# Kernel optimization log

Measured on AMD Instinct MI355X. Metric: run time of the kernel, lower is better.

## Reference

```python
import jax, jax.numpy as jnp
import numpy as np
import math

D_MODEL = 768
ED = 768           # d_inner = expand_factor * d_model = 768
N_STATE = 1        # ssm d_state
DT_RANK = math.ceil(D_MODEL / 16)  # 48
EPS = 1e-6


def setup_inputs() -> dict:
    key = jax.random.key(0)
    ks = jax.random.split(key, 12)
    s = lambda k, shape, scale: jax.random.normal(k, shape, dtype=jnp.float32) * scale
    x = jax.random.normal(ks[0], (8, 4096, D_MODEL), dtype=jnp.float32)
    return {
        "x": x,
        "rms_w": jnp.ones((D_MODEL,), jnp.float32),
        "in_proj_w": s(ks[1], (2 * ED, D_MODEL), 0.02),
        "conv_w": s(ks[2], (ED,), 0.5),          # depthwise conv, kernel=1 -> per-channel scale
        "conv_b": s(ks[3], (ED,), 0.02),
        "x_proj_w": s(ks[4], (DT_RANK + 2 * N_STATE, ED), 0.02),
        "dt_proj_w": s(ks[5], (ED, DT_RANK), 0.02),
        "dt_proj_b": s(ks[6], (ED,), 0.02),
        "A_log": jnp.log(jnp.tile(jnp.arange(1, N_STATE + 1, dtype=jnp.float32), (ED, 1))),  # (ED, N)
        "D": jnp.ones((ED,), jnp.float32),
        "out_proj_w": s(ks[7], (D_MODEL, ED), 0.02),
    }


def _selective_scan(xc, delta, A, Bm, C, D):
    # xc: (B,L,ED), delta: (B,L,ED), A: (ED,N), Bm: (B,L,N), C: (B,L,N)
    deltaA = jnp.exp(delta[..., None] * A)                      # (B,L,ED,N)
    deltaBx = delta[..., None] * Bm[:, :, None, :] * xc[..., None]  # (B,L,ED,N)

    def combine(left, right):
        a1, b1 = left
        a2, b2 = right
        return a1 * a2, a2 * b1 + b2

    _, hs = jax.lax.associative_scan(combine, (deltaA, deltaBx), axis=1)  # hs: (B,L,ED,N)
    y = jnp.einsum('blen,bln->ble', hs, C) + D * xc
    return y


def reference(x, rms_w, in_proj_w, conv_w, conv_b, x_proj_w, dt_proj_w,
              dt_proj_b, A_log, D, out_proj_w):
    # RMSNorm
    xn = x * jax.lax.rsqrt(jnp.mean(x * x, axis=-1, keepdims=True) + EPS) * rms_w

    # MambaBlock
    xz = xn @ in_proj_w.T                    # (B,L,2*ED)
    xc, z = jnp.split(xz, 2, axis=-1)
    # depthwise conv1d with kernel_size=1, padding=0 -> per-channel affine
    xc = jax.nn.silu(xc * conv_w + conv_b)

    dbc = xc @ x_proj_w.T                    # (B,L,dt_rank+2N)
    delta = dbc[..., :DT_RANK]
    Bm = dbc[..., DT_RANK:DT_RANK + N_STATE]
    C = dbc[..., DT_RANK + N_STATE:]
    delta = jax.nn.softplus(delta @ dt_proj_w.T + dt_proj_b)  # (B,L,ED)

    A = -jnp.exp(A_log)                      # (ED,N)
    y = _selective_scan(xc, delta, A, Bm, C, D)
    y = y * jax.nn.silu(z)
    return y @ out_proj_w.T                  # (B,L,D_MODEL)
```

## Files before the change

kernel.cpp:

```cpp
#include <hip/hip_runtime.h>

#define TOK   32768
#define DM    768
#define KDIM  768
#define LSEQ  4096
#define NC    64
#define CL    64
#define NCHAIN 6144

typedef __bf16 bf16x8 __attribute__((ext_vector_type(8)));
typedef float  f32x4  __attribute__((ext_vector_type(4)));
typedef unsigned short u16;
typedef unsigned int u32;

__device__ __forceinline__ u16 f2bf(float f) {
  unsigned u = __builtin_bit_cast(unsigned, f);
  u += 0x7fffu + ((u >> 16) & 1u);
  return (u16)(u >> 16);
}
__device__ __forceinline__ float bf2f(u32 h) {
  unsigned u = (h & 0xffffu) << 16;
  return __builtin_bit_cast(float, u);
}

#define GLOAD_LDS16(g, l) __builtin_amdgcn_global_load_lds( \
    (const __attribute__((address_space(1))) void*)(g),     \
    (__attribute__((address_space(3))) void*)(l), 16, 0, 0)

__global__ void cvt_k(const float* __restrict__ src, u16* __restrict__ dst, int n) {
  int i = blockIdx.x * 256 + threadIdx.x;
  if (i < n) dst[i] = f2bf(src[i]);
}

__global__ void cvt_pad_k(const float* __restrict__ src, u16* __restrict__ dst,
                          int rows, int cols, int dcols, int n) {
  int i = blockIdx.x * 256 + threadIdx.x;
  if (i >= n) return;
  int r = i / dcols, c = i % dcols;
  dst[i] = (r < rows && c < cols) ? f2bf(src[r * cols + c]) : (u16)0;
}

__global__ __launch_bounds__(192)
void rmsnorm_k(const float* __restrict__ x, const float* __restrict__ w,
               u16* __restrict__ xnb) {
  long t = blockIdx.x;
  int tid = threadIdx.x;
  float4 v = ((const float4*)x)[t * 192 + tid];
  float s = v.x * v.x + v.y * v.y + v.z * v.z + v.w * v.w;
#pragma unroll
  for (int o = 32; o; o >>= 1) s += __shfl_down(s, o, 64);
  __shared__ float red[3];
  if ((tid & 63) == 0) red[tid >> 6] = s;
  __syncthreads();
  float sc = rsqrtf((red[0] + red[1] + red[2]) * (1.f / 768.f) + 1e-6f);
  float4 ww = ((const float4*)w)[tid];
  ushort4 o;
  o.x = f2bf(v.x * sc * ww.x);
  o.y = f2bf(v.y * sc * ww.y);
  o.z = f2bf(v.z * sc * ww.z);
  o.w = f2bf(v.w * sc * ww.w);
  ((ushort4*)xnb)[t * 192 + tid] = o;
}

template <int EPI>
__global__ __launch_bounds__(256)
void gemm32(const u16* __restrict__ A, int lda,
            const u16* __restrict__ B, int ldb, int K,
            int GX, int RPX,
            float* __restrict__ C,
            const float* __restrict__ w0, const float* __restrict__ w1,
            u16* __restrict__ o0, u16* __restrict__ o1) {
  __shared__ __align__(16) u16 smA[2 * 4096];
  __shared__ __align__(16) u16 smB[2 * 4096];
  const int tid = threadIdx.x;
  const int lane = tid & 63;
  const int wid = tid >> 6;

  const int bid = blockIdx.x;
  const int xcd = bid & 7;
  const int p = bid >> 3;
  const int colp = p % GX;
  const int rowp = xcd * RPX + p / GX;
  const long rowBase = (long)rowp * 128;
  const long colBase = (long)colp * 128;

  const int wr = (wid >> 1) * 64;
  const int wc = (wid & 1) * 64;
  const int lr = lane & 15;
  const int kc = lane >> 4;
  const int kcs = kc ^ ((lr >> 1) & 3);

  const int c1 = tid + 256;
  const u16* gA0 = A + (rowBase + (tid >> 2)) * lda + ((tid & 3) ^ ((tid >> 3) & 3)) * 8;
  const u16* gA1 = A + (rowBase + (c1 >> 2)) * lda + ((c1 & 3) ^ ((c1 >> 3) & 3)) * 8;
  const u16* gB0 = B + (colBase + (tid >> 2)) * ldb + ((tid & 3) ^ ((tid >> 3) & 3)) * 8;
  const u16* gB1 = B + (colBase + (c1 >> 2)) * ldb + ((c1 & 3) ^ ((c1 >> 3) & 3)) * 8;

  f32x4 acc[4][4] = {};
  const int NT = K >> 5;

  auto STAGE = [&](int buf, int kt) {
    u16* bA = smA + buf * 4096;
    u16* bB = smB + buf * 4096;
    GLOAD_LDS16(gA0 + kt, &bA[tid * 8]);
    GLOAD_LDS16(gA1 + kt, &bA[c1 * 8]);
    GLOAD_LDS16(gB0 + kt, &bB[tid * 8]);
    GLOAD_LDS16(gB1 + kt, &bB[c1 * 8]);
  };

  STAGE(0, 0);
  __syncthreads();

  for (int t = 0; t < NT; ++t) {
    if (t + 1 < NT) STAGE((t + 1) & 1, (t + 1) << 5);
    const u16* cA = smA + (t & 1) * 4096;
    const u16* cB = smB + (t & 1) * 4096;
    bf16x8 af[4], bfr[4];
#pragma unroll
    for (int m = 0; m < 4; ++m)
      af[m] = *(const bf16x8*)&cA[(wr + m * 16 + lr) * 32 + kcs * 8];
#pragma unroll
    for (int n = 0; n < 4; ++n)
      bfr[n] = *(const bf16x8*)&cB[(wc + n * 16 + lr) * 32 + kcs * 8];
#pragma unroll
    for (int m = 0; m < 4; ++m)
#pragma unroll
      for (int n = 0; n < 4; ++n)
        acc[m][n] = __builtin_amdgcn_mfma_f32_16x16x32_bf16(af[m], bfr[n], acc[m][n], 0, 0, 0);
    __syncthreads();
  }

#pragma unroll
  for (int m = 0; m < 4; ++m)
#pragma unroll
    for (int n = 0; n < 4; ++n)
#pragma unroll
      for (int j = 0; j < 4; ++j) {
        long grow = rowBase + wr + m * 16 + kc * 4 + j;
        long gcol = colBase + wc + n * 16 + lr;
        float v = acc[m][n][j];
        if (EPI == 0) {
          C[grow * DM + gcol] = v;
        } else if (EPI == 1) {
          if (gcol < DM) {
            float t = v * w0[gcol] + w1[gcol];
            o0[grow * DM + gcol] = f2bf(t / (1.f + __expf(-t)));
          } else {
            o1[grow * DM + (gcol - DM)] = f2bf(v / (1.f + __expf(-v)));
          }
        } else if (EPI == 2) {
          float t = v + w0[gcol];
          float d = (t > 20.f) ? t : __logf(1.f + __expf(t));
          o0[grow * DM + gcol] = f2bf(d);
        } else {
          if (gcol < 64) o0[grow * 64 + gcol] = f2bf(v);
          if (gcol == 48) C[grow * 2 + 0] = v;
          if (gcol == 49) C[grow * 2 + 1] = v;
        }
      }
}

__global__ __launch_bounds__(384)
void scan1_k(const u16* __restrict__ deltab, const u16* __restrict__ xcb,
             const float* __restrict__ bmc, const float* __restrict__ A_log,
             float* __restrict__ aprod, float* __restrict__ hend) {
  int pe = threadIdx.x;
  int b = blockIdx.x, c = blockIdx.y;
  int e0 = pe * 2;
  float Ae0 = -__expf(A_log[e0]), Ae1 = -__expf(A_log[e0 + 1]);
  float ap0 = 1.f, h0 = 0.f, ap1 = 1.f, h1 = 0.f;
  long base = (long)b * LSEQ + (long)c * CL;
  for (int i = 0; i < CL; ++i) {
    long t = base + i;
    u32 dv = *(const u32*)&deltab[t * DM + e0];
    u32 xv = *(const u32*)&xcb[t * DM + e0];
    float Bm = bmc[t * 2];
    float d0 = bf2f(dv), d1 = bf2f(dv >> 16);
    float x0 = bf2f(xv), x1 = bf2f(xv >> 16);
    float a0 = __expf(d0 * Ae0), a1 = __expf(d1 * Ae1);
    ap0 *= a0; h0 = a0 * h0 + d0 * Bm * x0;
    ap1 *= a1; h1 = a1 * h1 + d1 * Bm * x1;
  }
  long chain = (long)c * NCHAIN + b * DM + e0;
  *(float2*)&aprod[chain] = make_float2(ap0, ap1);
  *(float2*)&hend[chain]  = make_float2(h0, h1);
}

__global__ __launch_bounds__(256)
void scan2_k(const float* __restrict__ aprod, const float* __restrict__ hend,
             float* __restrict__ carry) {
  int chain = blockIdx.x * 256 + threadIdx.x;
  float h = 0.f;
  for (int c = 0; c < NC; ++c) {
    carry[c * NCHAIN + chain] = h;
    h = aprod[c * NCHAIN + chain] * h + hend[c * NCHAIN + chain];
  }
}

__global__ __launch_bounds__(384)
void scan3_k(const u16* __restrict__ deltab, const u16* __restrict__ xcb,
             const float* __restrict__ bmc, const float* __restrict__ A_log,
             const float* __restrict__ Dp, const u16* __restrict__ szb,
             const float* __restrict__ carry, u16* __restrict__ ybf) {
  int pe = threadIdx.x;
  int b = blockIdx.x, c = blockIdx.y;
  int e0 = pe * 2;
  float Ae0 = -__expf(A_log[e0]), Ae1 = -__expf(A_log[e0 + 1]);
  float De0 = Dp[e0], De1 = Dp[e0 + 1];
  long chain = (long)c * NCHAIN + b * DM + e0;
  float2 hc = *(const float2*)&carry[chain];
  float h0 = hc.x, h1 = hc.y;
  long base = (long)b * LSEQ + (long)c * CL;
  for (int i = 0; i < CL; ++i) {
    long t = base + i;
    u32 dv = *(const u32*)&deltab[t * DM + e0];
    u32 xv = *(const u32*)&xcb[t * DM + e0];
    u32 sv = *(const u32*)&szb[t * DM + e0];
    float Bm = bmc[t * 2], Cc = bmc[t * 2 + 1];
    float d0 = bf2f(dv), d1 = bf2f(dv >> 16);
    float x0 = bf2f(xv), x1 = bf2f(xv >> 16);
    float a0 = __expf(d0 * Ae0), a1 = __expf(d1 * Ae1);
    h0 = a0 * h0 + d0 * Bm * x0;
    h1 = a1 * h1 + d1 * Bm * x1;
    float y0 = (h0 * Cc + De0 * x0) * bf2f(sv);
    float y1 = (h1 * Cc + De1 * x1) * bf2f(sv >> 16);
    *(u32*)&ybf[t * DM + e0] = (u32)f2bf(y0) | ((u32)f2bf(y1) << 16);
  }
}

extern "C" void kernel_launch(void* const* d_in, const int* in_sizes, int n_in,
                              void* d_out, int out_size, void* d_ws, size_t ws_size,
                              hipStream_t stream) {
  const float* x         = (const float*)d_in[0];
  const float* rms_w     = (const float*)d_in[1];
  const float* in_proj_w = (const float*)d_in[2];
  const float* conv_w    = (const float*)d_in[3];
  const float* conv_b    = (const float*)d_in[4];
  const float* x_proj_w  = (const float*)d_in[5];
  const float* dt_proj_w = (const float*)d_in[6];
  const float* dt_proj_b = (const float*)d_in[7];
  const float* A_log     = (const float*)d_in[8];
  const float* Dp        = (const float*)d_in[9];
  const float* out_proj_w= (const float*)d_in[10];
  float* out = (float*)d_out;

  char* ws = (char*)d_ws;
  size_t off = 0;
  auto alloc = [&](size_t bytes) -> void* {
    void* p = ws + off;
    off += (bytes + 255) & ~(size_t)255;
    return p;
  };
  u16*   xnb    = (u16*)alloc((size_t)TOK * DM * 2);
  u16*   xcb    = (u16*)alloc((size_t)TOK * DM * 2);
  u16*   szb    = (u16*)alloc((size_t)TOK * DM * 2);
  u16*   ybf    = (u16*)alloc((size_t)TOK * DM * 2);
  u16*   deltab = (u16*)alloc((size_t)TOK * DM * 2);
  u16*   dbcb   = (u16*)alloc((size_t)TOK * 64 * 2);
  float* bmc    = (float*)alloc((size_t)TOK * 2 * 4);
  u16*   wInB   = (u16*)alloc((size_t)1536 * 768 * 2);
  u16*   wXpB   = (u16*)alloc((size_t)128 * 768 * 2);
  u16*   wDtB   = (u16*)alloc((size_t)768 * 64 * 2);
  u16*   wOutB  = (u16*)alloc((size_t)768 * 768 * 2);
  float* aprod  = (float*)alloc((size_t)NC * NCHAIN * 4);
  float* hend   = (float*)alloc((size_t)NC * NCHAIN * 4);
  float* carry  = (float*)alloc((size_t)NC * NCHAIN * 4);

  cvt_k<<<(1536 * 768 + 255) / 256, 256, 0, stream>>>(in_proj_w, wInB, 1536 * 768);
  cvt_k<<<(768 * 768 + 255) / 256, 256, 0, stream>>>(out_proj_w, wOutB, 768 * 768);
  cvt_pad_k<<<(128 * 768 + 255) / 256, 256, 0, stream>>>(x_proj_w, wXpB, 50, 768, 768, 128 * 768);
  cvt_pad_k<<<(768 * 64 + 255) / 256, 256, 0, stream>>>(dt_proj_w, wDtB, 768, 48, 64, 768 * 64);

  rmsnorm_k<<<TOK, 192, 0, stream>>>(x, rms_w, xnb);

  gemm32<1><<<3072, 256, 0, stream>>>(
      xnb, DM, wInB, DM, KDIM, 12, 32, nullptr, conv_w, conv_b, xcb, szb);

  gemm32<3><<<256, 256, 0, stream>>>(
      xcb, DM, wXpB, DM, KDIM, 1, 32, bmc, nullptr, nullptr, dbcb, nullptr);

  gemm32<2><<<1536, 256, 0, stream>>>(
      dbcb, 64, wDtB, 64, 64, 6, 32, nullptr, dt_proj_b, nullptr, deltab, nullptr);

  scan1_k<<<dim3(8, NC), 384, 0, stream>>>(deltab, xcb, bmc, A_log, aprod, hend);
  scan2_k<<<NCHAIN / 256, 256, 0, stream>>>(aprod, hend, carry);
  scan3_k<<<dim3(8, NC), 384, 0, stream>>>(deltab, xcb, bmc, A_log, Dp, szb, carry, ybf);

  gemm32<0><<<1536, 256, 0, stream>>>(
      ybf, DM, wOutB, DM, KDIM, 6, 32, out, nullptr, nullptr, nullptr, nullptr);
}
```

Measured before the change: 343.9 us.

## Replace 4-wave GEMM with single-wave 64x64 tiles and barrier-free pipelining

Rewrites the shared GEMM kernel so each block is one 64-thread wavefront computing a 64x64 tile, not four waves on a 128x128 tile. Because a single wave owns its LDS tiles, __syncthreads is dropped and replaced with explicit vmcnt/lgkmcnt waits. Loads are issued two k-steps ahead, with the next stage overwriting the buffer just read. This removes block-level barrier stalls and adds parallelism, at the cost of less data reuse per tile (more global/L2 traffic) and many more small blocks. The grid sizes for all four GEMM launches are rescaled to match.

```diff
diff --git a/kernel.cpp b/kernel.cpp
--- a/kernel.cpp
+++ b/kernel.cpp
@@ -63,71 +63,66 @@
 }
 
 template <int EPI>
-__global__ __launch_bounds__(256)
-void gemm32(const u16* __restrict__ A, int lda,
-            const u16* __restrict__ B, int ldb, int K,
-            int GX, int RPX,
-            float* __restrict__ C,
-            const float* __restrict__ w0, const float* __restrict__ w1,
-            u16* __restrict__ o0, u16* __restrict__ o1) {
-  __shared__ __align__(16) u16 smA[2 * 4096];
-  __shared__ __align__(16) u16 smB[2 * 4096];
-  const int tid = threadIdx.x;
-  const int lane = tid & 63;
-  const int wid = tid >> 6;
-
+__global__ __launch_bounds__(64)
+void gemmw(const u16* __restrict__ A, int lda,
+           const u16* __restrict__ B, int ldb, int K,
+           int GX, int RPX,
+           float* __restrict__ C,
+           const float* __restrict__ w0, const float* __restrict__ w1,
+           u16* __restrict__ o0, u16* __restrict__ o1) {
+  __shared__ __align__(16) u16 smA[2 * 2048];
+  __shared__ __align__(16) u16 smB[2 * 2048];
+  const int l = threadIdx.x;
   const int bid = blockIdx.x;
   const int xcd = bid & 7;
   const int p = bid >> 3;
-  const int colp = p % GX;
-  const int rowp = xcd * RPX + p / GX;
-  const long rowBase = (long)rowp * 128;
-  const long colBase = (long)colp * 128;
-
-  const int wr = (wid >> 1) * 64;
-  const int wc = (wid & 1) * 64;
-  const int lr = lane & 15;
-  const int kc = lane >> 4;
+  const long rowBase = (long)(xcd * RPX + p / GX) * 64;
+  const long colBase = (long)(p % GX) * 64;
+
+  const int lr = l & 15;
+  const int kc = l >> 4;
   const int kcs = kc ^ ((lr >> 1) & 3);
 
-  const int c1 = tid + 256;
-  const u16* gA0 = A + (rowBase + (tid >> 2)) * lda + ((tid & 3) ^ ((tid >> 3) & 3)) * 8;
-  const u16* gA1 = A + (rowBase + (c1 >> 2)) * lda + ((c1 & 3) ^ ((c1 >> 3) & 3)) * 8;
-  const u16* gB0 = B + (colBase + (tid >> 2)) * ldb + ((tid & 3) ^ ((tid >> 3) & 3)) * 8;
-  const u16* gB1 = B + (colBase + (c1 >> 2)) * ldb + ((c1 & 3) ^ ((c1 >> 3) & 3)) * 8;
+  const int srow = l >> 2;
+  const int sslot = (l & 3) ^ ((l >> 3) & 3);
+  const u16* gA = A + (rowBase + srow) * lda + sslot * 8;
+  const u16* gB = B + (colBase + srow) * ldb + sslot * 8;
 
   f32x4 acc[4][4] = {};
   const int NT = K >> 5;
 
   auto STAGE = [&](int buf, int kt) {
-    u16* bA = smA + buf * 4096;
-    u16* bB = smB + buf * 4096;
-    GLOAD_LDS16(gA0 + kt, &bA[tid * 8]);
-    GLOAD_LDS16(gA1 + kt, &bA[c1 * 8]);
-    GLOAD_LDS16(gB0 + kt, &bB[tid * 8]);
-    GLOAD_LDS16(gB1 + kt, &bB[c1 * 8]);
+    u16* bA = smA + buf * 2048;
+    u16* bB = smB + buf * 2048;
+#pragma unroll
+    for (int i = 0; i < 4; ++i) {
+      GLOAD_LDS16(gA + (long)(16 * i) * lda + kt, &bA[(l + 64 * i) * 8]);
+      GLOAD_LDS16(gB + (long)(16 * i) * ldb + kt, &bB[(l + 64 * i) * 8]);
+    }
   };
 
   STAGE(0, 0);
-  __syncthreads();
+  if (NT > 1) STAGE(1, 32);
 
   for (int t = 0; t < NT; ++t) {
-    if (t + 1 < NT) STAGE((t + 1) & 1, (t + 1) << 5);
-    const u16* cA = smA + (t & 1) * 4096;
-    const u16* cB = smB + (t & 1) * 4096;
+    if (t + 1 < NT) asm volatile("s_waitcnt vmcnt(8)" ::: "memory");
+    else            asm volatile("s_waitcnt vmcnt(0)" ::: "memory");
+    const u16* cA = smA + (t & 1) * 2048;
+    const u16* cB = smB + (t & 1) * 2048;
     bf16x8 af[4], bfr[4];
 #pragma unroll
     for (int m = 0; m < 4; ++m)
-      af[m] = *(const bf16x8*)&cA[(wr + m * 16 + lr) * 32 + kcs * 8];
+      af[m] = *(const bf16x8*)&cA[(m * 16 + lr) * 32 + kcs * 8];
 #pragma unroll
     for (int n = 0; n < 4; ++n)
-      bfr[n] = *(const bf16x8*)&cB[(wc + n * 16 + lr) * 32 + kcs * 8];
+      bfr[n] = *(const bf16x8*)&cB[(n * 16 + lr) * 32 + kcs * 8];
+    asm volatile("s_waitcnt lgkmcnt(0)" ::: "memory");
+    if (t + 2 < NT) STAGE(t & 1, (t + 2) << 5);
 #pragma unroll
     for (int m = 0; m < 4; ++m)
 #pragma unroll
       for (int n = 0; n < 4; ++n)
         acc[m][n] = __builtin_amdgcn_mfma_f32_16x16x32_bf16(af[m], bfr[n], acc[m][n], 0, 0, 0);
-    __syncthreads();
   }
 
 #pragma unroll
@@ -136,24 +131,24 @@
     for (int n = 0; n < 4; ++n)
 #pragma unroll
       for (int j = 0; j < 4; ++j) {
-        long grow = rowBase + wr + m * 16 + kc * 4 + j;
-        long gcol = colBase + wc + n * 16 + lr;
+        long grow = rowBase + m * 16 + kc * 4 + j;
+        long gcol = colBase + n * 16 + lr;
         float v = acc[m][n][j];
         if (EPI == 0) {
           C[grow * DM + gcol] = v;
         } else if (EPI == 1) {
           if (gcol < DM) {
-            float t = v * w0[gcol] + w1[gcol];
-            o0[grow * DM + gcol] = f2bf(t / (1.f + __expf(-t)));
+            float t2 = v * w0[gcol] + w1[gcol];
+            o0[grow * DM + gcol] = f2bf(t2 / (1.f + __expf(-t2)));
           } else {
             o1[grow * DM + (gcol - DM)] = f2bf(v / (1.f + __expf(-v)));
           }
         } else if (EPI == 2) {
-          float t = v + w0[gcol];
-          float d = (t > 20.f) ? t : __logf(1.f + __expf(t));
+          float t2 = v + w0[gcol];
+          float d = (t2 > 20.f) ? t2 : __logf(1.f + __expf(t2));
           o0[grow * DM + gcol] = f2bf(d);
         } else {
-          if (gcol < 64) o0[grow * 64 + gcol] = f2bf(v);
+          o0[grow * 64 + gcol] = f2bf(v);
           if (gcol == 48) C[grow * 2 + 0] = v;
           if (gcol == 49) C[grow * 2 + 1] = v;
         }
@@ -273,19 +268,19 @@
 
   rmsnorm_k<<<TOK, 192, 0, stream>>>(x, rms_w, xnb);
 
-  gemm32<1><<<3072, 256, 0, stream>>>(
-      xnb, DM, wInB, DM, KDIM, 12, 32, nullptr, conv_w, conv_b, xcb, szb);
-
-  gemm32<3><<<256, 256, 0, stream>>>(
-      xcb, DM, wXpB, DM, KDIM, 1, 32, bmc, nullptr, nullptr, dbcb, nullptr);
-
-  gemm32<2><<<1536, 256, 0, stream>>>(
-      dbcb, 64, wDtB, 64, 64, 6, 32, nullptr, dt_proj_b, nullptr, deltab, nullptr);
+  gemmw<1><<<12288, 64, 0, stream>>>(
+      xnb, DM, wInB, DM, KDIM, 24, 64, nullptr, conv_w, conv_b, xcb, szb);
+
+  gemmw<3><<<512, 64, 0, stream>>>(
+      xcb, DM, wXpB, DM, KDIM, 1, 64, bmc, nullptr, nullptr, dbcb, nullptr);
+
+  gemmw<2><<<6144, 64, 0, stream>>>(
+      dbcb, 64, wDtB, 64, 64, 12, 64, nullptr, dt_proj_b, nullptr, deltab, nullptr);
 
   scan1_k<<<dim3(8, NC), 384, 0, stream>>>(deltab, xcb, bmc, A_log, aprod, hend);
   scan2_k<<<NCHAIN / 256, 256, 0, stream>>>(aprod, hend, carry);
   scan3_k<<<dim3(8, NC), 384, 0, stream>>>(deltab, xcb, bmc, A_log, Dp, szb, carry, ybf);
 
-  gemm32<0><<<1536, 256, 0, stream>>>(
-      ybf, DM, wOutB, DM, KDIM, 6, 32, out, nullptr, nullptr, nullptr, nullptr);
-}
+  gemmw<0><<<6144, 64, 0, stream>>>(
+      ybf, DM, wOutB, DM, KDIM, 12, 64, out, nullptr, nullptr, nullptr, nullptr);
+}
```

After: 411.4 us. 19.6% more time.
